# Kernel tuning notes

Measured on AMD Instinct MI355X. Metric: run time of the kernel, lower is better.

Reference implementation:

```python
import jax, jax.numpy as jnp
import numpy as np

N_NODES = 40000
N_EDGES = 640000
IN_DIM = 128
HIDDEN = 128
OUT_DIM = 64
N_GRAPHS = 64


def setup_inputs() -> dict:
    key = jax.random.key(0)
    ks = jax.random.split(key, 10)
    x = jax.random.normal(ks[0], (N_NODES, IN_DIM), dtype=jnp.float32)
    edge_index = jax.random.randint(ks[1], (2, N_EDGES), 0, N_NODES, dtype=jnp.int64)
    batch = jnp.sort(jax.random.randint(ks[2], (N_NODES,), 0, N_GRAPHS, dtype=jnp.int64))
    # GCNConv params (PyG: glorot weight, zero bias; random here for testing)
    s1 = 1.0 / np.sqrt(IN_DIM)
    s2 = 1.0 / np.sqrt(HIDDEN)
    W1 = jax.random.uniform(ks[3], (IN_DIM, HIDDEN), jnp.float32, -s1, s1)
    b1 = jax.random.uniform(ks[4], (HIDDEN,), jnp.float32, -s1, s1)
    W2 = jax.random.uniform(ks[5], (HIDDEN, HIDDEN), jnp.float32, -s2, s2)
    b2 = jax.random.uniform(ks[6], (HIDDEN,), jnp.float32, -s2, s2)
    Wl = jax.random.uniform(ks[7], (HIDDEN, OUT_DIM), jnp.float32, -s2, s2)
    bl = jax.random.uniform(ks[8], (OUT_DIM,), jnp.float32, -s2, s2)
    return {"x": x, "W1": W1, "b1": b1, "W2": W2, "b2": b2,
            "Wl": Wl, "bl": bl, "edge_index": edge_index, "batch": batch}


def gcn_conv(x, W, b, src, dst, num_nodes):
    # PyG GCNConv: transform, then symmetric-normalized aggregation with self-loops.
    h = x @ W  # [N, H]
    # degree of (A + I): in-degree at dst plus 1 for the self-loop
    deg = jax.ops.segment_sum(jnp.ones_like(dst, dtype=h.dtype), dst,
                              num_segments=num_nodes) + 1.0
    dinv = jax.lax.rsqrt(deg)  # deg >= 1 always
    norm = dinv[src] * dinv[dst]  # [E]
    agg = jax.ops.segment_sum(h[src] * norm[:, None], dst, num_segments=num_nodes)
    # self-loop contribution: norm_ii = dinv_i^2
    out = agg + (dinv * dinv)[:, None] * h
    return out + b


def reference(x, W1, b1, W2, b2, Wl, bl, edge_index, batch):
    src, dst = edge_index[0], edge_index[1]
    h = jax.nn.relu(gcn_conv(x, W1, b1, src, dst, N_NODES))
    h = jax.nn.relu(gcn_conv(h, W2, b2, src, dst, N_NODES))
    # global_mean_pool
    sums = jax.ops.segment_sum(h, batch, num_segments=N_GRAPHS)  # [G, H]
    cnts = jax.ops.segment_sum(jnp.ones((h.shape[0],), h.dtype), batch,
                               num_segments=N_GRAPHS)
    g = sums / jnp.maximum(cnts, 1.0)[:, None]
    g = g @ Wl + bl
    # F.normalize(p=2, dim=1): x / max(||x||, eps)
    nrm = jnp.linalg.norm(g, axis=1, keepdims=True)
    return g / jnp.maximum(nrm, 1e-12)
```

## Files before the change

### kernel.cpp

```cpp
#include <hip/hip_runtime.h>
#include <hip/hip_bf16.h>

#define N_NODES 40000
#define N_EDGES 640000
#define IN_DIM 128
#define HIDDEN 128
#define OUT_DIM 64
#define N_GRAPHS 64
#define CAP 64

__device__ inline unsigned int pack_bf2(float a, float b) {
  unsigned int ua = __float_as_uint(a);
  ua = ua + 0x7fffu + ((ua >> 16) & 1u);
  unsigned int ub = __float_as_uint(b);
  ub = ub + 0x7fffu + ((ub >> 16) & 1u);
  return (ua >> 16) | (ub & 0xffff0000u);
}

__global__ __launch_bounds__(256) void scatter_bucket_kernel(
    const int* __restrict__ src, const int* __restrict__ dst,
    int* __restrict__ cnt, unsigned short* __restrict__ bucket) {
  int e = blockIdx.x * 256 + threadIdx.x;
  if (e >= N_EDGES) return;
  int d = dst[e];
  int s = src[e];
  int p = atomicAdd(&cnt[d], 1);
  if (p < CAP) bucket[(size_t)d * CAP + p] = (unsigned short)s;
}

__global__ __launch_bounds__(256) void dinv_kernel(
    const int* __restrict__ cnt, float* __restrict__ dinv) {
  int n = blockIdx.x * 256 + threadIdx.x;
  if (n < N_NODES) dinv[n] = rsqrtf((float)cnt[n] + 1.0f);
}

__global__ __launch_bounds__(256) void finalize_kernel(
    const int* __restrict__ cnt, const unsigned short* __restrict__ bucket,
    const float* __restrict__ dinv, unsigned int* __restrict__ bucket2) {
  int wave = threadIdx.x >> 6;
  int lane = threadIdx.x & 63;
  int n = blockIdx.x * 4 + wave;
  int ecnt = min(cnt[n], CAP);
  unsigned int v = 0;
  if (lane < ecnt) {
    int s = bucket[(size_t)n * CAP + lane];
    unsigned int d = __float_as_uint(dinv[s]);
    d = d + 0x7fffu + ((d >> 16) & 1u);
    v = (d & 0xffff0000u) | (unsigned int)s;
  }
  bucket2[(size_t)n * CAP + lane] = v;
}

__global__ __launch_bounds__(256) void gemm_kernel(
    const float* __restrict__ A, const float* __restrict__ W,
    unsigned int* __restrict__ C) {
  __shared__ float As[8][65];
  __shared__ float Bs[8][128];
  int t = threadIdx.x;
  int tx = t & 15;
  int ty = t >> 4;
  int rowBase = blockIdx.x * 64;

  float acc[4][8];
#pragma unroll
  for (int i = 0; i < 4; ++i)
#pragma unroll
    for (int j = 0; j < 8; ++j) acc[i][j] = 0.0f;

  int arow = t >> 2;
  int akk = (t & 3) * 2;
  int bkk = t >> 5;
  int bcol = (t & 31) * 4;

  const float* Aptr = A + (size_t)(rowBase + arow) * 128 + akk;

  for (int kb = 0; kb < 128; kb += 8) {
    float2 av = *(const float2*)(Aptr + kb);
    float4 bv = *(const float4*)(W + (kb + bkk) * 128 + bcol);
    As[akk][arow] = av.x;
    As[akk + 1][arow] = av.y;
    *(float4*)&Bs[bkk][bcol] = bv;
    __syncthreads();
#pragma unroll
    for (int kk = 0; kk < 8; ++kk) {
      float a[4], b[8];
#pragma unroll
      for (int i = 0; i < 4; ++i) a[i] = As[kk][ty * 4 + i];
#pragma unroll
      for (int j = 0; j < 8; ++j) b[j] = Bs[kk][tx * 8 + j];
#pragma unroll
      for (int i = 0; i < 4; ++i)
#pragma unroll
        for (int j = 0; j < 8; ++j) acc[i][j] = fmaf(a[i], b[j], acc[i][j]);
    }
    __syncthreads();
  }

#pragma unroll
  for (int i = 0; i < 4; ++i) {
    unsigned int* cp = C + (size_t)(rowBase + ty * 4 + i) * 64 + tx * 4;
    uint4 v;
    v.x = pack_bf2(acc[i][0], acc[i][1]);
    v.y = pack_bf2(acc[i][2], acc[i][3]);
    v.z = pack_bf2(acc[i][4], acc[i][5]);
    v.w = pack_bf2(acc[i][6], acc[i][7]);
    *(uint4*)cp = v;
  }
}

__global__ __launch_bounds__(256) void agg_relu_kernel(
    const unsigned int* __restrict__ h, const int* __restrict__ cnt,
    const unsigned int* __restrict__ bucket2,
    const float* __restrict__ dinv, const float* __restrict__ bias,
    float* __restrict__ out, const int* __restrict__ batch,
    float* __restrict__ sums, int pool) {
  int wave = threadIdx.x >> 6;
  int lane = threadIdx.x & 63;
  int n = blockIdx.x * 4 + wave;

  unsigned int ev = bucket2[(size_t)n * CAP + lane];
  int ecnt = min(cnt[n], CAP);
  float di = dinv[n];

  float accx = 0.0f, accy = 0.0f;
  int iters = (ecnt + 15) & ~15;
  for (int eb = 0; eb < iters; eb += 16) {
#pragma unroll
    for (int i = 0; i < 16; ++i) {
      int e = eb + i;
      unsigned int edge = __shfl(ev, e);
      int s = edge & 0xffffu;
      float nm = __uint_as_float(edge & 0xffff0000u) * di;
      unsigned int hv = h[(size_t)s * 64 + lane];
      float hx = __uint_as_float(hv << 16);
      float hy = __uint_as_float(hv & 0xffff0000u);
      accx = fmaf(hx, nm, accx);
      accy = fmaf(hy, nm, accy);
    }
  }

  float sl = di * di;
  unsigned int hsv = h[(size_t)n * 64 + lane];
  float hsx = __uint_as_float(hsv << 16);
  float hsy = __uint_as_float(hsv & 0xffff0000u);
  float2 bv = ((const float2*)bias)[lane];
  float vx = fmaxf(fmaf(sl, hsx, accx) + bv.x, 0.0f);
  float vy = fmaxf(fmaf(sl, hsy, accy) + bv.y, 0.0f);

  if (!pool) {
    float2 o = {vx, vy};
    ((float2*)out)[(size_t)n * 64 + lane] = o;
  } else {
    int g = batch[n];
    atomicAdd(&sums[g * 128 + 2 * lane], vx);
    atomicAdd(&sums[g * 128 + 2 * lane + 1], vy);
  }
}

__global__ __launch_bounds__(64) void head_kernel(
    const int* __restrict__ batch, const float* __restrict__ sums,
    const float* __restrict__ Wl, const float* __restrict__ bl,
    float* __restrict__ out) {
  int g = blockIdx.x;
  int j = threadIdx.x;
  __shared__ float gv[128];
  __shared__ int bnd[2];
  if (j < 2) {
    int v = g + j;
    int lo = 0, hi = N_NODES;
    while (lo < hi) {
      int m = (lo + hi) >> 1;
      if (batch[m] < v) lo = m + 1; else hi = m;
    }
    bnd[j] = lo;
  }
  __syncthreads();
  float c = fmaxf((float)(bnd[1] - bnd[0]), 1.0f);
  float inv = 1.0f / c;
  gv[j] = sums[g * 128 + j] * inv;
  gv[j + 64] = sums[g * 128 + 64 + j] * inv;
  __syncthreads();
  float acc = bl[j];
#pragma unroll 8
  for (int k = 0; k < 128; ++k) acc = fmaf(gv[k], Wl[k * 64 + j], acc);
  float ss = acc * acc;
#pragma unroll
  for (int d = 32; d > 0; d >>= 1) ss += __shfl_xor(ss, d);
  float nrm = sqrtf(ss);
  out[g * 64 + j] = acc / fmaxf(nrm, 1e-12f);
}

extern "C" void kernel_launch(void* const* d_in, const int* in_sizes, int n_in,
                              void* d_out, int out_size, void* d_ws, size_t ws_size,
                              hipStream_t stream) {
  const float* x  = (const float*)d_in[0];
  const float* W1 = (const float*)d_in[1];
  const float* b1 = (const float*)d_in[2];
  const float* W2 = (const float*)d_in[3];
  const float* b2 = (const float*)d_in[4];
  const float* Wl = (const float*)d_in[5];
  const float* bl = (const float*)d_in[6];
  const int* edge_index = (const int*)d_in[7];
  const int* batch = (const int*)d_in[8];
  float* out = (float*)d_out;

  const int* esrc_in = edge_index;
  const int* edst_in = edge_index + N_EDGES;

  char* p = (char*)d_ws;
  unsigned int* bufA = (unsigned int*)p;
  p += (size_t)N_NODES * 64 * 4;
  float* bufB = (float*)p;  p += (size_t)N_NODES * 128 * 4;
  int* cnt    = (int*)p;    p += (size_t)N_NODES * 4;
  float* sums = (float*)p;  p += (size_t)N_GRAPHS * 128 * 4;
  float* dinv = (float*)p;  p += (size_t)N_NODES * 4;
  unsigned short* bucket = (unsigned short*)p;
  p += (size_t)N_NODES * CAP * 2;
  unsigned int* bucket2 = (unsigned int*)p;
  p += (size_t)N_NODES * CAP * 4;

  hipMemsetAsync(cnt, 0, (size_t)N_NODES * 4 + (size_t)N_GRAPHS * 128 * 4,
                 stream);

  int ceilN = (N_NODES + 255) / 256;
  int ceilE = (N_EDGES + 255) / 256;

  scatter_bucket_kernel<<<ceilE, 256, 0, stream>>>(esrc_in, edst_in, cnt, bucket);
  dinv_kernel<<<ceilN, 256, 0, stream>>>(cnt, dinv);
  finalize_kernel<<<N_NODES / 4, 256, 0, stream>>>(cnt, bucket, dinv, bucket2);

  gemm_kernel<<<N_NODES / 64, 256, 0, stream>>>(x, W1, bufA);
  agg_relu_kernel<<<N_NODES / 4, 256, 0, stream>>>(
      bufA, cnt, bucket2, dinv, b1, bufB, batch, sums, 0);

  gemm_kernel<<<N_NODES / 64, 256, 0, stream>>>(bufB, W2, bufA);
  agg_relu_kernel<<<N_NODES / 4, 256, 0, stream>>>(
      bufA, cnt, bucket2, dinv, b2, nullptr, batch, sums, 1);

  head_kernel<<<N_GRAPHS, 64, 0, stream>>>(batch, sums, Wl, bl, out);
}
```

Measured before the change: 310.8 us.

## Store layer-1 activations as bf16 and batch gather loads in aggregation

The first aggregation now writes its ReLU output as packed bf16 instead of fp32, and a new GEMM variant reads these bf16 activations for the second layer. This halves the intermediate write and read traffic. The aggregation loop also issues all 16 gathered loads before the FMAs, uses readlane instead of shfl, and skips padded edges. Nontemporal loads and stores are added as cache hints. Precision drops for the layer-2 input, which adds rounding error.

```diff
diff --git a/kernel.cpp b/kernel.cpp
--- a/kernel.cpp
+++ b/kernel.cpp
@@ -51,7 +51,7 @@
   bucket2[(size_t)n * CAP + lane] = v;
 }
 
-__global__ __launch_bounds__(256) void gemm_kernel(
+__global__ __launch_bounds__(256) void gemm_f32_kernel(
     const float* __restrict__ A, const float* __restrict__ W,
     unsigned int* __restrict__ C) {
   __shared__ float As[8][65];
@@ -108,34 +108,98 @@
   }
 }
 
+__global__ __launch_bounds__(256) void gemm_bf16_kernel(
+    const unsigned int* __restrict__ A, const float* __restrict__ W,
+    unsigned int* __restrict__ C) {
+  __shared__ float As[8][65];
+  __shared__ float Bs[8][128];
+  int t = threadIdx.x;
+  int tx = t & 15;
+  int ty = t >> 4;
+  int rowBase = blockIdx.x * 64;
+
+  float acc[4][8];
+#pragma unroll
+  for (int i = 0; i < 4; ++i)
+#pragma unroll
+    for (int j = 0; j < 8; ++j) acc[i][j] = 0.0f;
+
+  int arow = t >> 2;
+  int akk = (t & 3) * 2;
+  int bkk = t >> 5;
+  int bcol = (t & 31) * 4;
+
+  const unsigned int* Aptr = A + (size_t)(rowBase + arow) * 64 + (akk >> 1);
+
+  for (int kb = 0; kb < 128; kb += 8) {
+    unsigned int av = __builtin_nontemporal_load(Aptr + (kb >> 1));
+    float4 bv = *(const float4*)(W + (kb + bkk) * 128 + bcol);
+    As[akk][arow] = __uint_as_float(av << 16);
+    As[akk + 1][arow] = __uint_as_float(av & 0xffff0000u);
+    *(float4*)&Bs[bkk][bcol] = bv;
+    __syncthreads();
+#pragma unroll
+    for (int kk = 0; kk < 8; ++kk) {
+      float a[4], b[8];
+#pragma unroll
+      for (int i = 0; i < 4; ++i) a[i] = As[kk][ty * 4 + i];
+#pragma unroll
+      for (int j = 0; j < 8; ++j) b[j] = Bs[kk][tx * 8 + j];
+#pragma unroll
+      for (int i = 0; i < 4; ++i)
+#pragma unroll
+        for (int j = 0; j < 8; ++j) acc[i][j] = fmaf(a[i], b[j], acc[i][j]);
+    }
+    __syncthreads();
+  }
+
+#pragma unroll
+  for (int i = 0; i < 4; ++i) {
+    unsigned int* cp = C + (size_t)(rowBase + ty * 4 + i) * 64 + tx * 4;
+    uint4 v;
+    v.x = pack_bf2(acc[i][0], acc[i][1]);
+    v.y = pack_bf2(acc[i][2], acc[i][3]);
+    v.z = pack_bf2(acc[i][4], acc[i][5]);
+    v.w = pack_bf2(acc[i][6], acc[i][7]);
+    *(uint4*)cp = v;
+  }
+}
+
 __global__ __launch_bounds__(256) void agg_relu_kernel(
     const unsigned int* __restrict__ h, const int* __restrict__ cnt,
     const unsigned int* __restrict__ bucket2,
     const float* __restrict__ dinv, const float* __restrict__ bias,
-    float* __restrict__ out, const int* __restrict__ batch,
+    unsigned int* __restrict__ outb, const int* __restrict__ batch,
     float* __restrict__ sums, int pool) {
   int wave = threadIdx.x >> 6;
   int lane = threadIdx.x & 63;
   int n = blockIdx.x * 4 + wave;
 
-  unsigned int ev = bucket2[(size_t)n * CAP + lane];
+  unsigned int ev =
+      __builtin_nontemporal_load(&bucket2[(size_t)n * CAP + lane]);
   int ecnt = min(cnt[n], CAP);
   float di = dinv[n];
 
   float accx = 0.0f, accy = 0.0f;
-  int iters = (ecnt + 15) & ~15;
-  for (int eb = 0; eb < iters; eb += 16) {
+  for (int eb = 0; eb < ecnt; eb += 16) {
+    unsigned int hv[16];
+    float nmv[16];
 #pragma unroll
     for (int i = 0; i < 16; ++i) {
+      hv[i] = 0u;
+      nmv[i] = 0.0f;
       int e = eb + i;
-      unsigned int edge = __shfl(ev, e);
-      int s = edge & 0xffffu;
-      float nm = __uint_as_float(edge & 0xffff0000u) * di;
-      unsigned int hv = h[(size_t)s * 64 + lane];
-      float hx = __uint_as_float(hv << 16);
-      float hy = __uint_as_float(hv & 0xffff0000u);
-      accx = fmaf(hx, nm, accx);
-      accy = fmaf(hy, nm, accy);
+      if (e < ecnt) {
+        unsigned int edge = __builtin_amdgcn_readlane(ev, e);
+        int s = (int)(edge & 0xffffu);
+        nmv[i] = __uint_as_float(edge & 0xffff0000u) * di;
+        hv[i] = h[(size_t)s * 64 + lane];
+      }
+    }
+#pragma unroll
+    for (int i = 0; i < 16; ++i) {
+      accx = fmaf(__uint_as_float(hv[i] << 16), nmv[i], accx);
+      accy = fmaf(__uint_as_float(hv[i] & 0xffff0000u), nmv[i], accy);
     }
   }
 
@@ -148,8 +212,8 @@
   float vy = fmaxf(fmaf(sl, hsy, accy) + bv.y, 0.0f);
 
   if (!pool) {
-    float2 o = {vx, vy};
-    ((float2*)out)[(size_t)n * 64 + lane] = o;
+    unsigned int o = pack_bf2(vx, vy);
+    __builtin_nontemporal_store(o, &outb[(size_t)n * 64 + lane]);
   } else {
     int g = batch[n];
     atomicAdd(&sums[g * 128 + 2 * lane], vx);
@@ -210,7 +274,8 @@
   char* p = (char*)d_ws;
   unsigned int* bufA = (unsigned int*)p;
   p += (size_t)N_NODES * 64 * 4;
-  float* bufB = (float*)p;  p += (size_t)N_NODES * 128 * 4;
+  unsigned int* bufB = (unsigned int*)p;
+  p += (size_t)N_NODES * 64 * 4;
   int* cnt    = (int*)p;    p += (size_t)N_NODES * 4;
   float* sums = (float*)p;  p += (size_t)N_GRAPHS * 128 * 4;
   float* dinv = (float*)p;  p += (size_t)N_NODES * 4;
@@ -229,11 +294,11 @@
   dinv_kernel<<<ceilN, 256, 0, stream>>>(cnt, dinv);
   finalize_kernel<<<N_NODES / 4, 256, 0, stream>>>(cnt, bucket, dinv, bucket2);
 
-  gemm_kernel<<<N_NODES / 64, 256, 0, stream>>>(x, W1, bufA);
+  gemm_f32_kernel<<<N_NODES / 64, 256, 0, stream>>>(x, W1, bufA);
   agg_relu_kernel<<<N_NODES / 4, 256, 0, stream>>>(
       bufA, cnt, bucket2, dinv, b1, bufB, batch, sums, 0);
 
-  gemm_kernel<<<N_NODES / 64, 256, 0, stream>>>(bufB, W2, bufA);
+  gemm_bf16_kernel<<<N_NODES / 64, 256, 0, stream>>>(bufB, W2, bufA);
   agg_relu_kernel<<<N_NODES / 4, 256, 0, stream>>>(
       bufA, cnt, bucket2, dinv, b2, nullptr, batch, sums, 1);
 
```

Result: slower. 349.8 us (+12.6%).

## Use bf16 MFMA for second GEMM, store layer-1 output as bf16, inline dinv

Applied to the files above, without the earlier changes.

The first aggregation now writes bf16-packed activations instead of fp32, which halves that write and the second GEMM's read. The second layer's GEMM becomes a bf16 MFMA kernel that uses a transposed bf16 copy of W2 prepared by a small kernel. The separate dinv kernel and buffer are removed; the rsqrt is recomputed inline in the finalize and aggregation kernels, and shfl is replaced with readlane plus nontemporal loads and stores. This adds bf16 rounding on the layer-1 output, and the MFMA kernel writes its output with scattered 16-bit stores.

```diff
diff --git a/kernel.cpp b/kernel.cpp
--- a/kernel.cpp
+++ b/kernel.cpp
@@ -9,6 +9,14 @@
 #define N_GRAPHS 64
 #define CAP 64
 
+typedef short bf16x8 __attribute__((ext_vector_type(8)));
+typedef float f32x4 __attribute__((ext_vector_type(4)));
+
+__device__ inline unsigned short bf16_1(float a) {
+  unsigned int ua = __float_as_uint(a);
+  ua = ua + 0x7fffu + ((ua >> 16) & 1u);
+  return (unsigned short)(ua >> 16);
+}
 __device__ inline unsigned int pack_bf2(float a, float b) {
   unsigned int ua = __float_as_uint(a);
   ua = ua + 0x7fffu + ((ua >> 16) & 1u);
@@ -28,15 +36,9 @@
   if (p < CAP) bucket[(size_t)d * CAP + p] = (unsigned short)s;
 }
 
-__global__ __launch_bounds__(256) void dinv_kernel(
-    const int* __restrict__ cnt, float* __restrict__ dinv) {
-  int n = blockIdx.x * 256 + threadIdx.x;
-  if (n < N_NODES) dinv[n] = rsqrtf((float)cnt[n] + 1.0f);
-}
-
 __global__ __launch_bounds__(256) void finalize_kernel(
     const int* __restrict__ cnt, const unsigned short* __restrict__ bucket,
-    const float* __restrict__ dinv, unsigned int* __restrict__ bucket2) {
+    unsigned int* __restrict__ bucket2) {
   int wave = threadIdx.x >> 6;
   int lane = threadIdx.x & 63;
   int n = blockIdx.x * 4 + wave;
@@ -44,14 +46,23 @@
   unsigned int v = 0;
   if (lane < ecnt) {
     int s = bucket[(size_t)n * CAP + lane];
-    unsigned int d = __float_as_uint(dinv[s]);
+    float dv = rsqrtf((float)cnt[s] + 1.0f);
+    unsigned int d = __float_as_uint(dv);
     d = d + 0x7fffu + ((d >> 16) & 1u);
     v = (d & 0xffff0000u) | (unsigned int)s;
   }
   bucket2[(size_t)n * CAP + lane] = v;
 }
 
-__global__ __launch_bounds__(256) void gemm_kernel(
+__global__ __launch_bounds__(256) void wprep_kernel(
+    const float* __restrict__ W, unsigned short* __restrict__ Wt) {
+  int idx = blockIdx.x * 256 + threadIdx.x;
+  int k = idx >> 7;
+  int n = idx & 127;
+  Wt[n * 128 + k] = bf16_1(W[k * 128 + n]);
+}
+
+__global__ __launch_bounds__(256) void gemm_f32_kernel(
     const float* __restrict__ A, const float* __restrict__ W,
     unsigned int* __restrict__ C) {
   __shared__ float As[8][65];
@@ -108,19 +119,64 @@
   }
 }
 
+__global__ __launch_bounds__(256) void gemm_mfma_kernel(
+    const unsigned int* __restrict__ A, const unsigned short* __restrict__ Wt,
+    unsigned int* __restrict__ C) {
+  int wave = threadIdx.x >> 6;
+  int lane = threadIdx.x & 63;
+  int rowBase = blockIdx.x * 64 + wave * 16;
+  int lr = lane & 15;
+  int lg = lane >> 4;
+
+  bf16x8 afrag[4];
+  const unsigned int* arow = A + (size_t)(rowBase + lr) * 64;
+#pragma unroll
+  for (int kb = 0; kb < 4; ++kb) {
+    uint4 av = *(const uint4*)(arow + kb * 16 + lg * 4);
+    afrag[kb] = *reinterpret_cast<const bf16x8*>(&av);
+  }
+
+  f32x4 acc[8];
+#pragma unroll
+  for (int nt = 0; nt < 8; ++nt) acc[nt] = (f32x4){0.f, 0.f, 0.f, 0.f};
+
+#pragma unroll
+  for (int nt = 0; nt < 8; ++nt) {
+    const unsigned short* wrow = Wt + (size_t)(nt * 16 + lr) * 128;
+#pragma unroll
+    for (int kb = 0; kb < 4; ++kb) {
+      bf16x8 bfrag = *reinterpret_cast<const bf16x8*>(wrow + kb * 32 + lg * 8);
+      acc[nt] = __builtin_amdgcn_mfma_f32_16x16x32_bf16(afrag[kb], bfrag,
+                                                        acc[nt], 0, 0, 0);
+    }
+  }
+
+  unsigned short* Cs = (unsigned short*)C;
+#pragma unroll
+  for (int nt = 0; nt < 8; ++nt) {
+#pragma unroll
+    for (int r = 0; r < 4; ++r) {
+      int row = rowBase + lg * 4 + r;
+      int col = nt * 16 + lr;
+      Cs[(size_t)row * 128 + col] = bf16_1(acc[nt][r]);
+    }
+  }
+}
+
 __global__ __launch_bounds__(256) void agg_relu_kernel(
     const unsigned int* __restrict__ h, const int* __restrict__ cnt,
-    const unsigned int* __restrict__ bucket2,
-    const float* __restrict__ dinv, const float* __restrict__ bias,
-    float* __restrict__ out, const int* __restrict__ batch,
+    const unsigned int* __restrict__ bucket2, const float* __restrict__ bias,
+    unsigned int* __restrict__ outb, const int* __restrict__ batch,
     float* __restrict__ sums, int pool) {
   int wave = threadIdx.x >> 6;
   int lane = threadIdx.x & 63;
   int n = blockIdx.x * 4 + wave;
 
-  unsigned int ev = bucket2[(size_t)n * CAP + lane];
-  int ecnt = min(cnt[n], CAP);
-  float di = dinv[n];
+  unsigned int ev =
+      __builtin_nontemporal_load(&bucket2[(size_t)n * CAP + lane]);
+  int rawc = cnt[n];
+  int ecnt = min(rawc, CAP);
+  float di = rsqrtf((float)rawc + 1.0f);
 
   float accx = 0.0f, accy = 0.0f;
   int iters = (ecnt + 15) & ~15;
@@ -128,14 +184,12 @@
 #pragma unroll
     for (int i = 0; i < 16; ++i) {
       int e = eb + i;
-      unsigned int edge = __shfl(ev, e);
-      int s = edge & 0xffffu;
+      unsigned int edge = __builtin_amdgcn_readlane(ev, e);
+      int s = (int)(edge & 0xffffu);
       float nm = __uint_as_float(edge & 0xffff0000u) * di;
       unsigned int hv = h[(size_t)s * 64 + lane];
-      float hx = __uint_as_float(hv << 16);
-      float hy = __uint_as_float(hv & 0xffff0000u);
-      accx = fmaf(hx, nm, accx);
-      accy = fmaf(hy, nm, accy);
+      accx = fmaf(__uint_as_float(hv << 16), nm, accx);
+      accy = fmaf(__uint_as_float(hv & 0xffff0000u), nm, accy);
     }
   }
 
@@ -148,8 +202,8 @@
   float vy = fmaxf(fmaf(sl, hsy, accy) + bv.y, 0.0f);
 
   if (!pool) {
-    float2 o = {vx, vy};
-    ((float2*)out)[(size_t)n * 64 + lane] = o;
+    unsigned int o = pack_bf2(vx, vy);
+    __builtin_nontemporal_store(o, &outb[(size_t)n * 64 + lane]);
   } else {
     int g = batch[n];
     atomicAdd(&sums[g * 128 + 2 * lane], vx);
@@ -210,32 +264,33 @@
   char* p = (char*)d_ws;
   unsigned int* bufA = (unsigned int*)p;
   p += (size_t)N_NODES * 64 * 4;
-  float* bufB = (float*)p;  p += (size_t)N_NODES * 128 * 4;
+  unsigned int* bufB = (unsigned int*)p;
+  p += (size_t)N_NODES * 64 * 4;
   int* cnt    = (int*)p;    p += (size_t)N_NODES * 4;
   float* sums = (float*)p;  p += (size_t)N_GRAPHS * 128 * 4;
-  float* dinv = (float*)p;  p += (size_t)N_NODES * 4;
   unsigned short* bucket = (unsigned short*)p;
   p += (size_t)N_NODES * CAP * 2;
   unsigned int* bucket2 = (unsigned int*)p;
   p += (size_t)N_NODES * CAP * 4;
+  unsigned short* Wt2 = (unsigned short*)p;
+  p += 128 * 128 * 2;
 
   hipMemsetAsync(cnt, 0, (size_t)N_NODES * 4 + (size_t)N_GRAPHS * 128 * 4,
                  stream);
 
-  int ceilN = (N_NODES + 255) / 256;
   int ceilE = (N_EDGES + 255) / 256;
 
   scatter_bucket_kernel<<<ceilE, 256, 0, stream>>>(esrc_in, edst_in, cnt, bucket);
-  dinv_kernel<<<ceilN, 256, 0, stream>>>(cnt, dinv);
-  finalize_kernel<<<N_NODES / 4, 256, 0, stream>>>(cnt, bucket, dinv, bucket2);
-
-  gemm_kernel<<<N_NODES / 64, 256, 0, stream>>>(x, W1, bufA);
+  wprep_kernel<<<64, 256, 0, stream>>>(W2, Wt2);
+  finalize_kernel<<<N_NODES / 4, 256, 0, stream>>>(cnt, bucket, bucket2);
+
+  gemm_f32_kernel<<<N_NODES / 64, 256, 0, stream>>>(x, W1, bufA);
   agg_relu_kernel<<<N_NODES / 4, 256, 0, stream>>>(
-      bufA, cnt, bucket2, dinv, b1, bufB, batch, sums, 0);
-
-  gemm_kernel<<<N_NODES / 64, 256, 0, stream>>>(bufB, W2, bufA);
+      bufA, cnt, bucket2, b1, bufB, batch, sums, 0);
+
+  gemm_mfma_kernel<<<N_NODES / 64, 256, 0, stream>>>(bufB, Wt2, bufA);
   agg_relu_kernel<<<N_NODES / 4, 256, 0, stream>>>(
-      bufA, cnt, bucket2, dinv, b2, nullptr, batch, sums, 1);
+      bufA, cnt, bucket2, b2, nullptr, batch, sums, 1);
 
   head_kernel<<<N_GRAPHS, 64, 0, stream>>>(batch, sums, Wl, bl, out);
 }
```

Result: faster. 300.2 us (-3.4%).
